# Performance work log

Hardware: AMD Instinct MI355X
Metric: run time of the kernel (lower is better)

The kernel has to match this reference:

```python
import math
import jax, jax.numpy as jnp
import numpy as np

LMAX = 6
F_ACT = 16   # f_out // 8, channels through SO3Activation
F_MID = 64   # f_out // 2
N_A, N_B, N_C = 16, 8, 16  # SO(3) Euler-angle grid (resolution=8 quadrature in beta)
SQRT2 = math.sqrt(2.0)     # normalize2mom factor for relu

# ---- Wigner-D machinery (numpy, setup-time constants; mirrors e3nn conventions) ----

def _su2_generators(j):
    m = np.arange(-j, j)
    raising = np.diag(-np.sqrt(j * (j + 1) - m * (m + 1)), k=-1).astype(complex)
    m = np.arange(-j + 1, j + 1)
    lowering = np.diag(np.sqrt(j * (j + 1) - m * (m - 1)), k=1).astype(complex)
    m = np.arange(-j, j + 1)
    return np.stack([0.5 * (raising + lowering), np.diag(1j * m), -0.5j * (raising - lowering)])

def _q_real(l):
    q = np.zeros((2 * l + 1, 2 * l + 1), dtype=complex)
    for m in range(-l, 0):
        q[l + m, l + abs(m)] = 2 ** -0.5
        q[l + m, l - abs(m)] = -1j * 2 ** -0.5
    q[l, l] = 1
    for m in range(1, l + 1):
        q[l + m, l + abs(m)] = (-1) ** m * 2 ** -0.5
        q[l + m, l - abs(m)] = 1j * (-1) ** m * 2 ** -0.5
    return (-1j) ** l * q

def _so3_generators(l):
    X = _su2_generators(l)
    Q = _q_real(l)
    return np.real(np.einsum('ij,njk,kl->nil', np.conj(Q.T), X, Q))

def _expm(A):
    w, V = np.linalg.eig(A.astype(complex))
    return np.real((V * np.exp(w)) @ np.linalg.inv(V))

def _wigner_prod_grid(lmax, a, b, c):
    # flat_wigner on a product Euler grid: D(a,b,g) = exp(a*Jy) exp(b*Jx) exp(g*Jy)
    blocks = []
    for l in range(lmax + 1):
        X = _so3_generators(l)
        Ea = np.stack([_expm(t * X[1]) for t in a])
        Eb = np.stack([_expm(t * X[0]) for t in b])
        Ec = np.stack([_expm(t * X[1]) for t in c])
        D = np.einsum('amn,bnp,cpq->abcmq', Ea, Eb, Ec)
        blocks.append((2 * l + 1) ** 0.5 * D.reshape(len(a) * len(b) * len(c), -1))
    return np.concatenate(blocks, -1)

def _flat_wigner_pts(lmax, a, b, c):
    blocks = []
    for l in range(lmax + 1):
        X = _so3_generators(l)
        D = np.stack([_expm(ai * X[1]) @ _expm(bi * X[0]) @ _expm(ci * X[1]) for ai, bi, ci in zip(a, b, c)])
        blocks.append((2 * l + 1) ** 0.5 * D.reshape(len(a), -1))
    return np.concatenate(blocks, -1)

def _c8_angles():
    # escnn rot2dOnR2(8) elements, transposed and embedded into 3x3 with z fixed
    th = 2 * np.pi * np.arange(8) / 8
    M = np.zeros((8, 3, 3))
    M[:, 0, 0] = np.cos(th); M[:, 0, 1] = np.sin(th)
    M[:, 1, 0] = -np.sin(th); M[:, 1, 1] = np.cos(th)
    M[:, 2, 2] = 1.0
    x = M @ np.array([0.0, 1.0, 0.0])
    b = np.arccos(np.clip(x[:, 1], -1, 1))
    a = np.arctan2(x[:, 0], x[:, 2])
    def my(t): c, s = np.cos(t), np.sin(t); return np.array([[c, 0, s], [0, 1, 0], [-s, 0, c]])
    def mx(t): c, s = np.cos(t), np.sin(t); return np.array([[1, 0, 0], [0, c, -s], [0, s, c]])
    g = np.array([np.arctan2(R[0, 2], R[0, 0]) for R in [(my(a[i]) @ mx(b[i])).T @ M[i] for i in range(8)]])
    return a, b, g

# ---- precomputed constants ----
_A = 2 * np.pi * np.arange(N_A) / N_A
_XB, _WB = np.polynomial.legendre.leggauss(N_B)
_B = np.arccos(_XB)
_C = 2 * np.pi * np.arange(N_C) / N_C
D_IN = jnp.asarray(_wigner_prod_grid(1, _A, _B, _C), jnp.float32)                 # (G, 10)
_QW = np.broadcast_to((_WB / 2.0)[None, :, None] / (N_A * N_C), (N_A, N_B, N_C)).reshape(-1)
D_OUTW = jnp.asarray(_wigner_prod_grid(LMAX, _A, _B, _C) * _QW[:, None], jnp.float32)  # (G, 455), quadrature folded in
C8W = jnp.asarray(_flat_wigner_pts(LMAX, *_c8_angles()), jnp.float32)             # (8, 455)


def setup_inputs() -> dict:
    key = jax.random.key(0)
    ks = jax.random.split(key, 16)
    inp = {
        'x': jax.random.normal(ks[0], (16, 32, 128, 455), jnp.float32),
        'trajectory': jax.random.normal(ks[1], (16, 32, 10), jnp.float32),
        'w1_l0': jax.random.normal(ks[2], (1, F_ACT, 1, 1), jnp.float32),
        'w1_l1': jax.random.normal(ks[3], (1, F_ACT, 3, 3), jnp.float32),
    }
    for l in range(LMAX + 1):
        d = 2 * l + 1
        inp[f'w2_l{l}'] = jax.random.normal(ks[4 + l], (F_ACT, F_MID, d, d), jnp.float32)
    return inp


def reference(x, trajectory, w1_l0, w1_l1, w2_l0, w2_l1, w2_l2, w2_l3, w2_l4, w2_l5, w2_l6):
    w2s = [w2_l0, w2_l1, w2_l2, w2_l3, w2_l4, w2_l5, w2_l6]
    b, t, _ = trajectory.shape
    # pack trajectory into irreps 1x0e + 3x1e: scalar is last input component
    ti = jnp.concatenate([trajectory[..., 9:10], trajectory[..., :9]], axis=-1)  # (b,t,10)
    # proj_1 (o3.Linear, f_in=1 -> f_out=16), per-l block mixing with 1/sqrt(f_in*mul_in)
    o0 = ti[:, :, None, 0:1] * w1_l0[0, :, 0, 0][None, None, :, None]            # (b,t,16,1)
    x1 = ti[..., 1:10].reshape(b, t, 3, 3)                                       # (mul=3, m=3)
    o1 = jnp.einsum('btum,guw->btgwm', x1, w1_l1[0]) * (3.0 ** -0.5)             # (b,t,16,3,3)
    feat = jnp.concatenate([o0, o1.reshape(b, t, F_ACT, 9)], axis=-1)            # (b,t,16,10)
    # SO3Activation: irreps -> SO(3) grid -> relu (2nd-moment normalized) -> irreps up to LMAX
    sig = jnp.einsum('btci,gi->btcg', feat, D_IN)                                # (b,t,16,G)
    sig = jax.nn.relu(sig) * SQRT2
    feat = jnp.einsum('btcg,gi->btci', sig, D_OUTW)                              # (b,t,16,455)
    # proj_2 (o3.Linear on so3_irreps(6), f 16->64), block-diagonal per l
    outs = []
    off = 0
    for l in range(LMAX + 1):
        d = 2 * l + 1
        blk = feat[..., off:off + d * d].reshape(b, t, F_ACT, d, d)
        o = jnp.einsum('btfum,fguw->btgwm', blk, w2s[l]) * ((F_ACT * d) ** -0.5)
        outs.append(o.reshape(b, t, F_MID, d * d))
        off += d * d
    traj_out = jnp.concatenate(outs, axis=-1)                                    # (b,t,64,455)
    # Wigner-D projection onto C8 group elements
    traj_c8 = jnp.einsum('btcj,ij->btci', traj_out, C8W)                         # (b,t,64,8)
    x_c8 = jnp.einsum('bhcj,ij->bhci', x, C8W)                                   # (b,h,128,8)
    return x_c8, traj_c8
```

## Files before the change

kernel.cpp:

```cpp
#include <hip/hip_runtime.h>
#include <hip/hip_bf16.h>
#include <math.h>


typedef __attribute__((ext_vector_type(8))) short bf16x8;
typedef __attribute__((ext_vector_type(4))) float f32x4;
typedef __attribute__((ext_vector_type(16))) float f32x16;

__device__ const int c_offs[8] = {0, 1, 10, 35, 84, 165, 286, 455};

struct SetupArgs {
  double angA[16];
  double angB[8];
  double c8a[8], c8b[8], c8g[8];
};
struct QWArgs { double wb[8]; };
struct W2Ptrs { const void* p[7]; };

__device__ __forceinline__ float bf2f(unsigned short u) {
  union { unsigned int i; float f; } v; v.i = ((unsigned int)u) << 16; return v.f;
}
__device__ __forceinline__ unsigned short f2bf(float f) {
  union { float f; unsigned int i; } v; v.f = f;
  unsigned int r = v.i + 0x7fffu + ((v.i >> 16) & 1u);
  return (unsigned short)(r >> 16);
}
__device__ __forceinline__ float in_val(const void* p, size_t i, int isf) {
  return isf ? ((const float*)p)[i] : bf2f(((const unsigned short*)p)[i]);
}
__device__ __forceinline__ void gl_lds16(const void* g, void* lds) {
  __builtin_amdgcn_global_load_lds(
      (const __attribute__((address_space(1))) unsigned int*)g,
      (__attribute__((address_space(3))) unsigned int*)lds, 16, 0, 0);
}

__global__ __launch_bounds__(192) void k_exps(SetupArgs args, double* exps,
                                              const void* x, int* flag) {
  __shared__ double Qr[169], Qi[169], Bm[169], R[169];
  __shared__ double coefA[13], coefB[13], rowsum[13];
  __shared__ double snorm;
  __shared__ int cnt;
  int tid = threadIdx.x;

  if (blockIdx.x == 336) {
    if (tid == 0) cnt = 0;
    __syncthreads();
    if (tid < 64) {
      float v = ((const float*)x)[tid];
      float a = fabsf(v);
      int ok = (v == v) && (a > 9.0949470e-13f) && (a < 1.0995116e12f);
      atomicAdd(&cnt, ok);
    }
    __syncthreads();
    if (tid == 0) *flag = (cnt >= 32) ? 1 : 0;
    return;
  }

  int l = blockIdx.x / 48, item = blockIdx.x % 48;
  int n = 2 * l + 1;
  int e = tid;
  bool val = (e < 169);
  int r = e / 13, c = e % 13;

  if (val) { Qr[e] = 0.0; Qi[e] = 0.0; }
  __syncthreads();
  if (tid == 0) {
    const double is2 = 0.70710678118654752440;
    for (int m = -l; m <= l; m++) {
      int rr = l + m;
      if (m < 0) {
        Qr[rr * 13 + (l - m)] = is2;
        Qi[rr * 13 + (l + m)] = -is2;
      } else if (m == 0) {
        Qr[l * 13 + l] = 1.0;
      } else {
        double s = (m & 1) ? -1.0 : 1.0;
        Qr[rr * 13 + (l + m)] = s * is2;
        Qi[rr * 13 + (l - m)] = s * is2;
      }
    }
  }
  double jj = (double)l;
  if (tid < 13) {
    double m1 = (double)(tid - 1 - l);
    coefA[tid] = -0.5 * sqrt(fmax(jj * (jj + 1.0) - m1 * (m1 + 1.0), 0.0));
    double m2 = (double)(tid + 1 - l);
    coefB[tid] = 0.5 * sqrt(fmax(jj * (jj + 1.0) - m2 * (m2 - 1.0), 0.0));
  }
  __syncthreads();
  {
    int lm = l & 3;
    double pr = (lm == 0) ? 1.0 : (lm == 2 ? -1.0 : 0.0);
    double pi = (lm == 1) ? -1.0 : (lm == 3 ? 1.0 : 0.0);
    if (val) {
      double qr = Qr[e], qi = Qi[e];
      Qr[e] = qr * pr - qi * pi;
      Qi[e] = qr * pi + qi * pr;
    }
  }
  __syncthreads();

  double t; int axis;
  if (item < 16)      { t = args.angA[item];      axis = 1; }
  else if (item < 24) { t = args.angB[item - 16]; axis = 0; }
  else if (item < 32) { t = args.c8a[item - 24];  axis = 1; }
  else if (item < 40) { t = args.c8b[item - 32];  axis = 0; }
  else                { t = args.c8g[item - 40];  axis = 1; }

  if (val) {
    double accr = 0.0;
    if (axis == 1) {
#pragma unroll
      for (int p = 0; p < 13; p++) {
        double mp = (double)(p - l);
        double ar = Qr[p * 13 + r], ai = -Qi[p * 13 + r];
        double br = Qr[p * 13 + c], bi = Qi[p * 13 + c];
        accr += -mp * (ar * bi + ai * br);
      }
    } else {
#pragma unroll
      for (int p = 0; p < 13; p++) {
        double xr = 0.0, xi = 0.0;
        if (p > 0) {
          double v = coefA[p];
          xr += v * Qr[(p - 1) * 13 + c]; xi += v * Qi[(p - 1) * 13 + c];
        }
        if (p < 12) {
          double v = coefB[p];
          xr += v * Qr[(p + 1) * 13 + c]; xi += v * Qi[(p + 1) * 13 + c];
        }
        double ar = Qr[p * 13 + r], ai = -Qi[p * 13 + r];
        accr += ar * xr - ai * xi;
      }
    }
    Bm[e] = t * accr;
  }
  __syncthreads();
  if (tid < 13) {
    double s = 0.0;
#pragma unroll
    for (int cc = 0; cc < 13; cc++) s += fabs(Bm[tid * 13 + cc]);
    rowsum[tid] = s;
  }
  __syncthreads();
  if (tid == 0) {
    double mx = 0.0;
#pragma unroll
    for (int rr = 0; rr < 13; rr++) mx = fmax(mx, rowsum[rr]);
    int s = 0;
    while (mx > 0.5 && s < 48) { mx *= 0.5; s++; }
    snorm = (double)s;
  }
  __syncthreads();
  int sq = (int)snorm;
  double sc = 1.0;
  for (int i = 0; i < sq; i++) sc *= 0.5;
  if (val) {
    double b = Bm[e] * sc;
    Bm[e] = b;
    R[e] = b / 16.0 + ((r == c) ? 1.0 : 0.0);
  }
  __syncthreads();
  for (int k = 15; k >= 1; k--) {
    double acc = 0.0;
    if (val) {
#pragma unroll
      for (int p = 0; p < 13; p++) acc += Bm[r * 13 + p] * R[p * 13 + c];
    }
    __syncthreads();
    if (val) R[e] = acc / (double)k + ((r == c) ? 1.0 : 0.0);
    __syncthreads();
  }
  for (int i = 0; i < sq; i++) {
    double acc = 0.0;
    if (val) {
#pragma unroll
      for (int p = 0; p < 13; p++) acc += R[r * 13 + p] * R[p * 13 + c];
    }
    __syncthreads();
    if (val) R[e] = acc;
    __syncthreads();
  }
  double* out = exps + (size_t)blockIdx.x * 169;
  if (val) out[e] = R[e];
  (void)n;
}

__global__ __launch_bounds__(192) void k_assemble(const double* exps, QWArgs qw,
                                                  unsigned short* dwt, float* dint,
                                                  float* c8w,
                                                  const void* traj, const void* w1l0,
                                                  const void* w1l1, float* feat,
                                                  const int* flag) {
  __shared__ double Ea[169], Eb[169], Ec[169], T1[169];
  int tid = threadIdx.x;
  int bx = blockIdx.x;

  if (bx >= 3640) {
    int isf = __builtin_amdgcn_readfirstlane(flag[0]);
    int idx = (bx - 3640) * 192 + tid;
    if (idx >= 512 * 160) return;
    int bt = idx / 160, rem = idx % 160;
    int c = rem / 10, i = rem % 10;
    float v;
    if (i == 0) {
      v = in_val(traj, bt * 10 + 9, isf) * in_val(w1l0, c, isf);
    } else {
      int ii = i - 1, w = ii / 3, m = ii % 3;
      float acc = 0.0f;
      for (int u = 0; u < 3; u++)
        acc += in_val(traj, bt * 10 + 3 * u + m, isf) *
               in_val(w1l1, c * 9 + u * 3 + w, isf);
      v = acc * 0.57735026918962576f;
    }
    feat[idx] = v;
    return;
  }

  int e = tid;
  bool valp = (e < 169);
  int r = e / 13, c = e % 13;

  if (bx >= 3584) {
    int idx = bx - 3584;
    int l = idx / 8, ci = idx % 8;
    int d = 2 * l + 1;
    const double* pa = exps + (size_t)(l * 48 + 24 + ci) * 169;
    const double* pb = exps + (size_t)(l * 48 + 32 + ci) * 169;
    const double* pc = exps + (size_t)(l * 48 + 40 + ci) * 169;
    if (valp) { Ea[e] = pa[e]; Eb[e] = pb[e]; Ec[e] = pc[e]; }
    __syncthreads();
    if (valp) {
      double acc = 0.0;
#pragma unroll
      for (int p = 0; p < 13; p++) acc += Ea[r * 13 + p] * Eb[p * 13 + c];
      T1[e] = acc;
    }
    __syncthreads();
    double scale = sqrt((double)(2 * l + 1));
    if (valp) {
      double acc = 0.0;
#pragma unroll
      for (int p = 0; p < 13; p++) acc += T1[r * 13 + p] * Ec[p * 13 + c];
      if (r < d && c < d)
        c8w[ci * 512 + c_offs[l] + r * d + c] = (float)(scale * acc);
    }
    if (l == 0) {
      for (int jz = 455 + tid; jz < 512; jz += 192)
        c8w[ci * 512 + jz] = 0.0f;
    }
    return;
  }

  int l = bx / 512, rem = bx % 512;
  int a = rem >> 5, b = (rem >> 2) & 7, cg = rem & 3;
  int d = 2 * l + 1;
  const double* pa = exps + (size_t)(l * 48 + a) * 169;
  const double* pb = exps + (size_t)(l * 48 + 16 + b) * 169;
  if (valp) { Ea[e] = pa[e]; Eb[e] = pb[e]; }
  __syncthreads();
  if (valp) {
    double acc = 0.0;
#pragma unroll
    for (int p = 0; p < 13; p++) acc += Ea[r * 13 + p] * Eb[p * 13 + c];
    T1[e] = acc;
  }
  double scale = sqrt((double)(2 * l + 1));
  double qwv = qw.wb[b] * (1.0 / 512.0);
  bool inblk = valp && (r < d) && (c < d);
  int j = inblk ? (c_offs[l] + r * d + c) : 0;
  const double* ctab = exps + (size_t)(l * 48) * 169;
  for (int cc = cg * 4; cc < cg * 4 + 4; cc++) {
    __syncthreads();
    if (valp) Ec[e] = ctab[(size_t)cc * 169 + e];
    __syncthreads();
    int g = a * 128 + b * 16 + cc;
    if (valp) {
      double acc = 0.0;
#pragma unroll
      for (int p = 0; p < 13; p++) acc += T1[r * 13 + p] * Ec[p * 13 + c];
      if (inblk) {
        dwt[(size_t)j * 2048 + g] = f2bf((float)(scale * acc * qwv));
        if (l == 1) dint[(size_t)(1 + r * 3 + c) * 2048 + g] = (float)(scale * acc);
        if (l == 0 && e == 0) dint[g] = (float)(scale * acc);
      }
    }
    if (l == 0) {
      for (int jz = 455 + tid; jz < 512; jz += 192)
        dwt[(size_t)jz * 2048 + g] = 0;
    }
  }
}

__global__ __launch_bounds__(256) void k_sig(const float* feat, const float* dint,
                                             unsigned short* sig) {
  int bi = blockIdx.x >> 3;
  int g = ((blockIdx.x & 7) << 8) + threadIdx.x;
  float din[10];
#pragma unroll
  for (int i = 0; i < 10; i++) din[i] = dint[(size_t)i * 2048 + g];
  const float* fr = feat + bi * 160;
  for (int cc = 0; cc < 16; cc++) {
    float acc = 0.0f;
#pragma unroll
    for (int i = 0; i < 10; i++) acc += fr[cc * 10 + i] * din[i];
    acc = fmaxf(acc, 0.0f) * 1.41421356237309505f;
    sig[(size_t)(bi * 16 + cc) * 2048 + g] = f2bf(acc);
  }
}

__global__ __launch_bounds__(256) void k_ebuild(W2Ptrs w2, const float* c8w,
                                                unsigned short* et, const int* flag) {
  int isf = __builtin_amdgcn_readfirstlane(flag[0]);
  int idx = blockIdx.x * 256 + threadIdx.x;
  int n = idx >> 13;
  int rest = idx & 8191;
  int f = rest >> 9, jj = rest & 511;
  size_t oaddr = (size_t)n * 8192 + f * 512 + jj;
  if (jj >= 455) { et[oaddr] = 0; return; }
  int l = 0;
  while (jj >= c_offs[l + 1]) l++;
  int d = 2 * l + 1;
  int rloc = jj - c_offs[l];
  int u = rloc / d, m = rloc % d;
  int g = n >> 3, i = n & 7;
  const void* wp = w2.p[l];
  float acc = 0.0f;
  for (int w = 0; w < d; w++) {
    float wv = in_val(wp, ((size_t)(f * 64 + g) * d + u) * d + w, isf);
    acc += wv * c8w[i * 512 + c_offs[l] + w * d + m];
  }
  acc *= rsqrtf((float)(16 * d));
  et[oaddr] = f2bf(acc);
}

__global__ __launch_bounds__(256) void k_gemm2(const unsigned short* A,
                                               const unsigned short* B,
                                               unsigned short* C) {
  __shared__ __align__(16) unsigned short As[128 * 64];
  __shared__ __align__(16) unsigned short Bs[64 * 64];
  int tid = threadIdx.x;
  int lane = tid & 63, wid = tid >> 6;
  int mt = blockIdx.x >> 3, nt = blockIdx.x & 7;
  int m0 = mt * 128, n0 = nt * 64;
  int wm = wid >> 1, wn = wid & 1;
  f32x16 acc[2];
#pragma unroll
  for (int t = 0; t < 2; t++)
#pragma unroll
    for (int r = 0; r < 16; r++) acc[t][r] = 0.0f;

  int r0 = tid >> 3;
  int kcl = (tid & 7) ^ (r0 & 7);
  const unsigned short* Abase = A + (size_t)m0 * 2048;
  const unsigned short* Bbase = B + (size_t)n0 * 2048;
  int mrow = (lane & 31);
  int xr = lane & 7;
  int khalf = lane >> 5;

  for (int kt = 0; kt < 32; kt++) {
    int k0 = kt * 64;
#pragma unroll
    for (int i = 0; i < 4; i++)
      gl_lds16(Abase + (size_t)(i * 32 + r0) * 2048 + k0 + kcl * 8,
               &As[i * 2048 + wid * 512]);
#pragma unroll
    for (int i = 0; i < 2; i++)
      gl_lds16(Bbase + (size_t)(i * 32 + r0) * 2048 + k0 + kcl * 8,
               &Bs[i * 2048 + wid * 512]);
    __syncthreads();
#pragma unroll
    for (int q = 0; q < 4; q++) {
      int qc = q * 2 + khalf;
      bf16x8 bv = *(const bf16x8*)&Bs[(wn * 32 + mrow) * 64 + (qc ^ xr) * 8];
#pragma unroll
      for (int t = 0; t < 2; t++) {
        bf16x8 av = *(const bf16x8*)&As[(wm * 64 + t * 32 + mrow) * 64 + (qc ^ xr) * 8];
        acc[t] = __builtin_amdgcn_mfma_f32_32x32x16_bf16(av, bv, acc[t], 0, 0, 0);
      }
    }
    __syncthreads();
  }
  int col = n0 + wn * 32 + (lane & 31);
#pragma unroll
  for (int t = 0; t < 2; t++)
#pragma unroll
    for (int r = 0; r < 16; r++) {
      int row = m0 + wm * 64 + t * 32 + (r & 3) + 8 * (r >> 2) + 4 * (lane >> 5);
      C[(size_t)row * 512 + col] = f2bf(acc[t][r]);
    }
}

__global__ __launch_bounds__(256) void k_gemm3(const unsigned short* A,
                                               const unsigned short* B, float* Cp) {
  __shared__ __align__(16) unsigned short As[64 * 32];
  __shared__ __align__(16) unsigned short Bs[128 * 32];
  int tid = threadIdx.x, lane = tid & 63, wid = tid >> 6;
  int kc = blockIdx.x >> 5;
  int mt = (blockIdx.x >> 2) & 7, nt = blockIdx.x & 3;
  int m0 = mt * 64, n0 = nt * 128;
  int wm = wid >> 1, wn = wid & 1;
  f32x4 acc[2][4];
#pragma unroll
  for (int a = 0; a < 2; a++)
#pragma unroll
    for (int b = 0; b < 4; b++) acc[a][b] = (f32x4){0.f, 0.f, 0.f, 0.f};
  int c0 = tid;
  int ar = c0 >> 2, ak = (c0 & 3) * 8;
  const unsigned short* Abase = A + (size_t)m0 * 8192 + kc * 1024;
  const unsigned short* Bbase = B + (size_t)n0 * 8192 + kc * 1024;
  int row = lane & 15, kq = (lane >> 4) * 8;
  for (int kt = 0; kt < 32; kt++) {
    int k0 = kt * 32;
    gl_lds16(Abase + (size_t)ar * 8192 + k0 + ak, &As[wid * 512]);
    gl_lds16(Bbase + (size_t)ar * 8192 + k0 + ak, &Bs[wid * 512]);
    gl_lds16(Bbase + (size_t)(ar + 64) * 8192 + k0 + ak, &Bs[2048 + wid * 512]);
    __syncthreads();
    bf16x8 af[2], bfr[4];
#pragma unroll
    for (int im = 0; im < 2; im++)
      af[im] = *(const bf16x8*)&As[(wm * 32 + im * 16 + row) * 32 + kq];
#pragma unroll
    for (int in = 0; in < 4; in++)
      bfr[in] = *(const bf16x8*)&Bs[(wn * 64 + in * 16 + row) * 32 + kq];
#pragma unroll
    for (int im = 0; im < 2; im++)
#pragma unroll
      for (int in = 0; in < 4; in++)
        acc[im][in] = __builtin_amdgcn_mfma_f32_16x16x32_bf16(af[im], bfr[in],
                                                              acc[im][in], 0, 0, 0);
    __syncthreads();
  }
  int col = lane & 15, rq = (lane >> 4) * 4;
  float* out = Cp + (size_t)kc * 262144;
#pragma unroll
  for (int im = 0; im < 2; im++)
#pragma unroll
    for (int in = 0; in < 4; in++)
#pragma unroll
      for (int r = 0; r < 4; r++) {
        int rr = m0 + wm * 32 + im * 16 + rq + r;
        int cc = n0 + wn * 64 + in * 16 + col;
        out[(size_t)rr * 512 + cc] = acc[im][in][r];
      }
}

__global__ __launch_bounds__(256) void k_xc8r(const void* x, const float* c8w,
                                              const float* Cp, void* dout,
                                              const int* flag) {
  int tid = threadIdx.x, lane = tid & 63, wid = tid >> 6;
  int isf = __builtin_amdgcn_readfirstlane(flag[0]);

  if (blockIdx.x >= 1024) {
    int idx = (blockIdx.x - 1024) * 256 + tid;
    const float4* c = (const float4*)Cp;
    float s0 = 0.f, s1 = 0.f, s2 = 0.f, s3 = 0.f;
#pragma unroll
    for (int p = 0; p < 8; p++) {
      float4 v = c[idx + p * 65536];
      s0 += v.x; s1 += v.y; s2 += v.z; s3 += v.w;
    }
    size_t base = 524288 + (size_t)idx * 4;
    if (isf) {
      float4 o; o.x = s0; o.y = s1; o.z = s2; o.w = s3;
      *(float4*)((float*)dout + base) = o;
    } else {
      unsigned int p0 = (unsigned int)f2bf(s0) | ((unsigned int)f2bf(s1) << 16);
      unsigned int p1 = (unsigned int)f2bf(s2) | ((unsigned int)f2bf(s3) << 16);
      uint2 pk; pk.x = p0; pk.y = p1;
      *(uint2*)((unsigned short*)dout + base) = pk;
    }
    return;
  }

  int gw = blockIdx.x * 4 + wid;
  float cw[8][8];
#pragma unroll
  for (int t = 0; t < 8; t++)
#pragma unroll
    for (int i = 0; i < 8; i++)
      cw[t][i] = c8w[i * 512 + t * 64 + lane];
  const float* xf = (const float*)x;
  const unsigned short* xh = (const unsigned short*)x;
  for (int r = gw * 16; r < gw * 16 + 16; r++) {
    float acc[8];
#pragma unroll
    for (int i = 0; i < 8; i++) acc[i] = 0.0f;
    if (isf) {
      const float* xr = xf + (size_t)r * 455;
#pragma unroll
      for (int t = 0; t < 8; t++) {
        int j = t * 64 + lane;
        float xv = (j < 455) ? xr[j] : 0.0f;
#pragma unroll
        for (int i = 0; i < 8; i++) acc[i] += xv * cw[t][i];
      }
    } else {
      const unsigned short* xr = xh + (size_t)r * 455;
#pragma unroll
      for (int t = 0; t < 8; t++) {
        int j = t * 64 + lane;
        float xv = (j < 455) ? bf2f(xr[j]) : 0.0f;
#pragma unroll
        for (int i = 0; i < 8; i++) acc[i] += xv * cw[t][i];
      }
    }
#pragma unroll
    for (int off = 32; off >= 1; off >>= 1)
#pragma unroll
      for (int i = 0; i < 8; i++) acc[i] += __shfl_xor(acc[i], off);
    float v = acc[0];
    v = (lane == 1) ? acc[1] : v;
    v = (lane == 2) ? acc[2] : v;
    v = (lane == 3) ? acc[3] : v;
    v = (lane == 4) ? acc[4] : v;
    v = (lane == 5) ? acc[5] : v;
    v = (lane == 6) ? acc[6] : v;
    v = (lane == 7) ? acc[7] : v;
    if (lane < 8) {
      if (isf) ((float*)dout)[(size_t)r * 8 + lane] = v;
      else     ((unsigned short*)dout)[(size_t)r * 8 + lane] = f2bf(v);
    }
  }
}

extern "C" void kernel_launch(void* const* d_in, const int* in_sizes, int n_in,
                              void* d_out, int out_size, void* d_ws, size_t ws_size,
                              hipStream_t stream) {
  const void* x    = d_in[0];
  const void* traj = d_in[1];
  const void* w1l0 = d_in[2];
  const void* w1l1 = d_in[3];
  W2Ptrs w2;
  for (int l = 0; l < 7; l++) w2.p[l] = d_in[4 + l];

  char* ws = (char*)d_ws;
  double* exps          = (double*)(ws + 0);
  float* dint           = (float*)(ws + 458752);
  float* c8w            = (float*)(ws + 540672);
  unsigned short* dwt   = (unsigned short*)(ws + 573440);
  float* feat           = (float*)(ws + 2670592);
  unsigned short* sig   = (unsigned short*)(ws + 2998272);
  unsigned short* f2    = (unsigned short*)(ws + 36552704);
  unsigned short* et    = (unsigned short*)(ws + 44941312);
  float* cp             = (float*)(ws + 53329920);
  int* flag             = (int*)(ws + 61718528);

  SetupArgs sa; QWArgs qa;
  for (int i = 0; i < 16; i++) sa.angA[i] = 2.0 * M_PI * (double)i / 16.0;
  static const double XB[8] = {
    -0.9602898564975363, -0.7966664774136267, -0.5255324099163290,
    -0.1834346424956498,  0.1834346424956498,  0.5255324099163290,
     0.7966664774136267,  0.9602898564975363};
  static const double WBv[8] = {
     0.1012285362903763, 0.2223810344533745, 0.3137066458778873,
     0.3626837833783620, 0.3626837833783620, 0.3137066458778873,
     0.2223810344533745, 0.1012285362903763};
  for (int i = 0; i < 8; i++) { sa.angB[i] = acos(XB[i]); qa.wb[i] = WBv[i]; }
  for (int i = 0; i < 8; i++) {
    double th = 2.0 * M_PI * (double)i / 8.0;
    double Mm[3][3] = {{cos(th), sin(th), 0.0},
                       {-sin(th), cos(th), 0.0},
                       {0.0, 0.0, 1.0}};
    double x0 = Mm[0][1], x1 = Mm[1][1], x2 = Mm[2][1];
    double bb = acos(fmax(-1.0, fmin(1.0, x1)));
    double aa = atan2(x0, x2);
    double ca_ = cos(aa), sa_ = sin(aa), cb_ = cos(bb), sb_ = sin(bb);
    double MY[3][3] = {{ca_, 0, sa_}, {0, 1, 0}, {-sa_, 0, ca_}};
    double MX[3][3] = {{1, 0, 0}, {0, cb_, -sb_}, {0, sb_, cb_}};
    double P1[3][3], Rr[3][3];
    for (int r = 0; r < 3; r++)
      for (int c = 0; c < 3; c++) {
        double s = 0.0;
        for (int k = 0; k < 3; k++) s += MY[r][k] * MX[k][c];
        P1[r][c] = s;
      }
    for (int r = 0; r < 3; r++)
      for (int c = 0; c < 3; c++) {
        double s = 0.0;
        for (int k = 0; k < 3; k++) s += P1[k][r] * Mm[k][c];
        Rr[r][c] = s;
      }
    double gg = atan2(Rr[0][2], Rr[0][0]);
    sa.c8a[i] = aa; sa.c8b[i] = bb; sa.c8g[i] = gg;
  }

  k_exps<<<337, 192, 0, stream>>>(sa, exps, x, flag);
  k_assemble<<<4067, 192, 0, stream>>>(exps, qa, dwt, dint, c8w,
                                       traj, w1l0, w1l1, feat, flag);
  k_sig<<<4096, 256, 0, stream>>>(feat, dint, sig);
  k_ebuild<<<16384, 256, 0, stream>>>(w2, c8w, et, flag);
  k_gemm2<<<512, 256, 0, stream>>>(sig, dwt, f2);
  k_gemm3<<<256, 256, 0, stream>>>(f2, et, cp);
  k_xc8r<<<1280, 256, 0, stream>>>(x, c8w, cp, d_out, flag);
}
```

Before: 333.3 us.

## Double-buffer GEMM LDS loads, remap blocks, vectorize ebuild, refine xc8r reduction

Both bf16 GEMMs now use two LDS buffers: the next K-tile is fetched with global_load_lds while MFMAs run on the current one, and a single waitcnt plus barrier replaces the two syncthreads per iteration. gemm2 block indices are remapped so blocks on the same XCD share M tiles, and gemm3 changes its tile ordering. k_ebuild computes four outputs per thread with branch-free l/offset/division logic and writes them as one ushort4. k_xc8r halves rows per wave and reduces with a shorter shuffle tree, doubling its grid. The extra LDS buffers lower possible occupancy.

```diff
diff --git a/kernel.cpp b/kernel.cpp
--- a/kernel.cpp
+++ b/kernel.cpp
@@ -33,6 +33,9 @@
       (const __attribute__((address_space(1))) unsigned int*)g,
       (__attribute__((address_space(3))) unsigned int*)lds, 16, 0, 0);
 }
+__device__ __forceinline__ void wait_bar() {
+  asm volatile("s_waitcnt vmcnt(0)\n\ts_barrier" ::: "memory");
+}
 
 __global__ __launch_bounds__(192) void k_exps(SetupArgs args, double* exps,
                                               const void* x, int* flag) {
@@ -57,7 +60,6 @@
   }
 
   int l = blockIdx.x / 48, item = blockIdx.x % 48;
-  int n = 2 * l + 1;
   int e = tid;
   bool val = (e < 169);
   int r = e / 13, c = e % 13;
@@ -183,7 +185,6 @@
   }
   double* out = exps + (size_t)blockIdx.x * 169;
   if (val) out[e] = R[e];
-  (void)n;
 }
 
 __global__ __launch_bounds__(192) void k_assemble(const double* exps, QWArgs qw,
@@ -312,36 +313,54 @@
 __global__ __launch_bounds__(256) void k_ebuild(W2Ptrs w2, const float* c8w,
                                                 unsigned short* et, const int* flag) {
   int isf = __builtin_amdgcn_readfirstlane(flag[0]);
-  int idx = blockIdx.x * 256 + threadIdx.x;
-  int n = idx >> 13;
-  int rest = idx & 8191;
-  int f = rest >> 9, jj = rest & 511;
-  size_t oaddr = (size_t)n * 8192 + f * 512 + jj;
-  if (jj >= 455) { et[oaddr] = 0; return; }
-  int l = 0;
-  while (jj >= c_offs[l + 1]) l++;
-  int d = 2 * l + 1;
-  int rloc = jj - c_offs[l];
-  int u = rloc / d, m = rloc % d;
+  int base = (blockIdx.x * 256 + threadIdx.x) * 4;
+  int n = base >> 13;
+  int rest = base & 8191;
+  int f = rest >> 9, jj0 = rest & 511;
   int g = n >> 3, i = n & 7;
-  const void* wp = w2.p[l];
-  float acc = 0.0f;
-  for (int w = 0; w < d; w++) {
-    float wv = in_val(wp, ((size_t)(f * 64 + g) * d + u) * d + w, isf);
-    acc += wv * c8w[i * 512 + c_offs[l] + w * d + m];
-  }
-  acc *= rsqrtf((float)(16 * d));
-  et[oaddr] = f2bf(acc);
+  unsigned short ov[4];
+#pragma unroll
+  for (int s = 0; s < 4; s++) {
+    int jj = jj0 + s;
+    if (jj >= 455) { ov[s] = 0; continue; }
+    int l    = (jj >= 1) + (jj >= 10) + (jj >= 35) + (jj >= 84) +
+               (jj >= 165) + (jj >= 286);
+    int offs = jj >= 286 ? 286 : jj >= 165 ? 165 : jj >= 84 ? 84 :
+               jj >= 35 ? 35 : jj >= 10 ? 10 : jj >= 1 ? 1 : 0;
+    int mg   = jj >= 286 ? 20165 : jj >= 165 ? 23832 : jj >= 84 ? 29128 :
+               jj >= 35 ? 37450 : jj >= 10 ? 52429 : jj >= 1 ? 87382 : 262144;
+    int d = 2 * l + 1;
+    int rloc = jj - offs;
+    int u = (rloc * mg) >> 18;
+    int m = rloc - u * d;
+    const void* wp = w2.p[0];
+    wp = (l >= 1) ? w2.p[1] : wp;
+    wp = (l >= 2) ? w2.p[2] : wp;
+    wp = (l >= 3) ? w2.p[3] : wp;
+    wp = (l >= 4) ? w2.p[4] : wp;
+    wp = (l >= 5) ? w2.p[5] : wp;
+    wp = (l >= 6) ? w2.p[6] : wp;
+    float acc = 0.0f;
+    for (int w = 0; w < d; w++) {
+      float wv = in_val(wp, ((size_t)(f * 64 + g) * d + u) * d + w, isf);
+      acc += wv * c8w[i * 512 + offs + w * d + m];
+    }
+    acc *= rsqrtf((float)(16 * d));
+    ov[s] = f2bf(acc);
+  }
+  *(ushort4*)&et[(size_t)n * 8192 + f * 512 + jj0] =
+      make_ushort4(ov[0], ov[1], ov[2], ov[3]);
 }
 
 __global__ __launch_bounds__(256) void k_gemm2(const unsigned short* A,
                                                const unsigned short* B,
                                                unsigned short* C) {
-  __shared__ __align__(16) unsigned short As[128 * 64];
-  __shared__ __align__(16) unsigned short Bs[64 * 64];
+  __shared__ __align__(16) unsigned short As[2][128 * 64];
+  __shared__ __align__(16) unsigned short Bs[2][64 * 64];
   int tid = threadIdx.x;
   int lane = tid & 63, wid = tid >> 6;
-  int mt = blockIdx.x >> 3, nt = blockIdx.x & 7;
+  int xcd = blockIdx.x & 7, bi = blockIdx.x >> 3;
+  int mt = xcd * 8 + (bi >> 3), nt = bi & 7;
   int m0 = mt * 128, n0 = nt * 64;
   int wm = wid >> 1, wn = wid & 1;
   f32x16 acc[2];
@@ -358,28 +377,34 @@
   int xr = lane & 7;
   int khalf = lane >> 5;
 
-  for (int kt = 0; kt < 32; kt++) {
+  auto STAGE = [&](int buf, int kt) {
     int k0 = kt * 64;
 #pragma unroll
     for (int i = 0; i < 4; i++)
       gl_lds16(Abase + (size_t)(i * 32 + r0) * 2048 + k0 + kcl * 8,
-               &As[i * 2048 + wid * 512]);
+               &As[buf][i * 2048 + wid * 512]);
 #pragma unroll
     for (int i = 0; i < 2; i++)
       gl_lds16(Bbase + (size_t)(i * 32 + r0) * 2048 + k0 + kcl * 8,
-               &Bs[i * 2048 + wid * 512]);
-    __syncthreads();
+               &Bs[buf][i * 2048 + wid * 512]);
+  };
+
+  STAGE(0, 0);
+  wait_bar();
+  int cur = 0;
+  for (int kt = 0; kt < 32; kt++) {
+    if (kt < 31) STAGE(cur ^ 1, kt + 1);
 #pragma unroll
     for (int q = 0; q < 4; q++) {
       int qc = q * 2 + khalf;
-      bf16x8 bv = *(const bf16x8*)&Bs[(wn * 32 + mrow) * 64 + (qc ^ xr) * 8];
+      bf16x8 bv = *(const bf16x8*)&Bs[cur][(wn * 32 + mrow) * 64 + (qc ^ xr) * 8];
 #pragma unroll
       for (int t = 0; t < 2; t++) {
-        bf16x8 av = *(const bf16x8*)&As[(wm * 64 + t * 32 + mrow) * 64 + (qc ^ xr) * 8];
+        bf16x8 av = *(const bf16x8*)&As[cur][(wm * 64 + t * 32 + mrow) * 64 + (qc ^ xr) * 8];
         acc[t] = __builtin_amdgcn_mfma_f32_32x32x16_bf16(av, bv, acc[t], 0, 0, 0);
       }
     }
-    __syncthreads();
+    if (kt < 31) { wait_bar(); cur ^= 1; }
   }
   int col = n0 + wn * 32 + (lane & 31);
 #pragma unroll
@@ -393,11 +418,10 @@
 
 __global__ __launch_bounds__(256) void k_gemm3(const unsigned short* A,
                                                const unsigned short* B, float* Cp) {
-  __shared__ __align__(16) unsigned short As[64 * 32];
-  __shared__ __align__(16) unsigned short Bs[128 * 32];
+  __shared__ __align__(16) unsigned short As[2][64 * 32];
+  __shared__ __align__(16) unsigned short Bs[2][128 * 32];
   int tid = threadIdx.x, lane = tid & 63, wid = tid >> 6;
-  int kc = blockIdx.x >> 5;
-  int mt = (blockIdx.x >> 2) & 7, nt = blockIdx.x & 3;
+  int mt = blockIdx.x >> 5, kc = (blockIdx.x >> 2) & 7, nt = blockIdx.x & 3;
   int m0 = mt * 64, n0 = nt * 128;
   int wm = wid >> 1, wn = wid & 1;
   f32x4 acc[2][4];
@@ -405,31 +429,37 @@
   for (int a = 0; a < 2; a++)
 #pragma unroll
     for (int b = 0; b < 4; b++) acc[a][b] = (f32x4){0.f, 0.f, 0.f, 0.f};
-  int c0 = tid;
-  int ar = c0 >> 2, ak = (c0 & 3) * 8;
+  int ar = tid >> 2, ak = (tid & 3) * 8;
   const unsigned short* Abase = A + (size_t)m0 * 8192 + kc * 1024;
   const unsigned short* Bbase = B + (size_t)n0 * 8192 + kc * 1024;
   int row = lane & 15, kq = (lane >> 4) * 8;
+
+  auto STAGE = [&](int buf, int kt) {
+    int k0 = kt * 32;
+    gl_lds16(Abase + (size_t)ar * 8192 + k0 + ak, &As[buf][wid * 512]);
+    gl_lds16(Bbase + (size_t)ar * 8192 + k0 + ak, &Bs[buf][wid * 512]);
+    gl_lds16(Bbase + (size_t)(ar + 64) * 8192 + k0 + ak, &Bs[buf][2048 + wid * 512]);
+  };
+
+  STAGE(0, 0);
+  wait_bar();
+  int cur = 0;
   for (int kt = 0; kt < 32; kt++) {
-    int k0 = kt * 32;
-    gl_lds16(Abase + (size_t)ar * 8192 + k0 + ak, &As[wid * 512]);
-    gl_lds16(Bbase + (size_t)ar * 8192 + k0 + ak, &Bs[wid * 512]);
-    gl_lds16(Bbase + (size_t)(ar + 64) * 8192 + k0 + ak, &Bs[2048 + wid * 512]);
-    __syncthreads();
+    if (kt < 31) STAGE(cur ^ 1, kt + 1);
     bf16x8 af[2], bfr[4];
 #pragma unroll
     for (int im = 0; im < 2; im++)
-      af[im] = *(const bf16x8*)&As[(wm * 32 + im * 16 + row) * 32 + kq];
+      af[im] = *(const bf16x8*)&As[cur][(wm * 32 + im * 16 + row) * 32 + kq];
 #pragma unroll
     for (int in = 0; in < 4; in++)
-      bfr[in] = *(const bf16x8*)&Bs[(wn * 64 + in * 16 + row) * 32 + kq];
+      bfr[in] = *(const bf16x8*)&Bs[cur][(wn * 64 + in * 16 + row) * 32 + kq];
 #pragma unroll
     for (int im = 0; im < 2; im++)
 #pragma unroll
       for (int in = 0; in < 4; in++)
         acc[im][in] = __builtin_amdgcn_mfma_f32_16x16x32_bf16(af[im], bfr[in],
                                                               acc[im][in], 0, 0, 0);
-    __syncthreads();
+    if (kt < 31) { wait_bar(); cur ^= 1; }
   }
   int col = lane & 15, rq = (lane >> 4) * 4;
   float* out = Cp + (size_t)kc * 262144;
@@ -451,8 +481,8 @@
   int tid = threadIdx.x, lane = tid & 63, wid = tid >> 6;
   int isf = __builtin_amdgcn_readfirstlane(flag[0]);
 
-  if (blockIdx.x >= 1024) {
-    int idx = (blockIdx.x - 1024) * 256 + tid;
+  if (blockIdx.x >= 2048) {
+    int idx = (blockIdx.x - 2048) * 256 + tid;
     const float4* c = (const float4*)Cp;
     float s0 = 0.f, s1 = 0.f, s2 = 0.f, s3 = 0.f;
 #pragma unroll
@@ -482,7 +512,7 @@
       cw[t][i] = c8w[i * 512 + t * 64 + lane];
   const float* xf = (const float*)x;
   const unsigned short* xh = (const unsigned short*)x;
-  for (int r = gw * 16; r < gw * 16 + 16; r++) {
+  for (int r = gw * 8; r < gw * 8 + 8; r++) {
     float acc[8];
 #pragma unroll
     for (int i = 0; i < 8; i++) acc[i] = 0.0f;
@@ -506,17 +536,21 @@
       }
     }
 #pragma unroll
-    for (int off = 32; off >= 1; off >>= 1)
+    for (int off = 1; off <= 4; off <<= 1)
 #pragma unroll
       for (int i = 0; i < 8; i++) acc[i] += __shfl_xor(acc[i], off);
+    int lg = lane & 7;
     float v = acc[0];
-    v = (lane == 1) ? acc[1] : v;
-    v = (lane == 2) ? acc[2] : v;
-    v = (lane == 3) ? acc[3] : v;
-    v = (lane == 4) ? acc[4] : v;
-    v = (lane == 5) ? acc[5] : v;
-    v = (lane == 6) ? acc[6] : v;
-    v = (lane == 7) ? acc[7] : v;
+    v = (lg == 1) ? acc[1] : v;
+    v = (lg == 2) ? acc[2] : v;
+    v = (lg == 3) ? acc[3] : v;
+    v = (lg == 4) ? acc[4] : v;
+    v = (lg == 5) ? acc[5] : v;
+    v = (lg == 6) ? acc[6] : v;
+    v = (lg == 7) ? acc[7] : v;
+    v += __shfl_xor(v, 8);
+    v += __shfl_xor(v, 16);
+    v += __shfl_xor(v, 32);
     if (lane < 8) {
       if (isf) ((float*)dout)[(size_t)r * 8 + lane] = v;
       else     ((unsigned short*)dout)[(size_t)r * 8 + lane] = f2bf(v);
@@ -589,8 +623,8 @@
   k_assemble<<<4067, 192, 0, stream>>>(exps, qa, dwt, dint, c8w,
                                        traj, w1l0, w1l1, feat, flag);
   k_sig<<<4096, 256, 0, stream>>>(feat, dint, sig);
-  k_ebuild<<<16384, 256, 0, stream>>>(w2, c8w, et, flag);
+  k_ebuild<<<4096, 256, 0, stream>>>(w2, c8w, et, flag);
   k_gemm2<<<512, 256, 0, stream>>>(sig, dwt, f2);
   k_gemm3<<<256, 256, 0, stream>>>(f2, et, cp);
-  k_xc8r<<<1280, 256, 0, stream>>>(x, c8w, cp, d_out, flag);
-}
+  k_xc8r<<<2304, 256, 0, stream>>>(x, c8w, cp, d_out, flag);
+}
```

Result: no change. 328.2 us (-1.5%).
